# Performance work log

Hardware: AMD Instinct MI355X
Metric: run time of the kernel (lower is better)

## Reference

```python
import jax, jax.numpy as jnp
import numpy as np

NUM_SAMPLES = 4096
TAU = 0.07
EPS = 1e-20


def setup_inputs() -> dict:
    key = jax.random.key(0)
    flows = jax.random.normal(key, (32, 2, 512, 512), dtype=jnp.float32)
    return {"flows": flows}


def reference(flows):
    # flows: [b, 2, h, w]
    b, _, h, w = flows.shape
    hw = h * w
    # sampling weights: L2 norm over the 2 flow components, scaled by 1/tau
    dist = jnp.sqrt(jnp.sum(flows * flows, axis=1)) / TAU  # [b, h, w]
    dist = dist.reshape(b, hw)  # [b, h*w]
    # torch.multinomial(dist, k) without replacement == Gumbel-top-k on log-weights
    logits = jnp.log(dist + EPS)
    g = jax.random.gumbel(jax.random.key(42), (b, hw), dtype=flows.dtype)
    _, indices = jax.lax.top_k(logits + g, NUM_SAMPLES)  # [b, num_samples] int32
    # scatter-based mask (equivalent to one_hot(indices).max(dim=1), without the
    # huge [b, num_samples, h*w] intermediate)
    batch_idx = jnp.arange(b)[:, None]  # [b, 1]
    flat_masks = jnp.zeros((b, hw), dtype=flows.dtype).at[batch_idx, indices].set(1.0)
    masks = flat_masks.reshape(b, 1, h, w)  # [b, 1, h, w]
    sparse_output = masks * flows  # [b, 2, h, w]
    sparse_output = jnp.concatenate([sparse_output, masks], axis=1)  # [b, 3, h, w]
    return sparse_output, indices, masks
```

## Files before the change

kernel.cpp:

```cpp
#include <hip/hip_runtime.h>
#include <stdint.h>

#define HW 262144
#define NB 32
#define TOPK 4096
#define NTOTAL (NB * HW)
#define GBLK 4096
#define CBLK 32768

#define OUT_BYTES 134742016ull

#define OFF_WIN 33554432
#define OFF_HA  35651584
#define OFF_HB  37748736
#define OFF_STA 39845888
#define OFF_STT 39846144
#define OFF_FLG 39846272
#define OFF_CNT 39846400

__device__ __forceinline__ uint32_t rotl32(uint32_t x, int d) {
  return (x << d) | (x >> (32 - d));
}

__device__ __forceinline__ void threefry2x32_k42(uint32_t x0, uint32_t x1,
                                                 uint32_t& o0, uint32_t& o1) {
  const uint32_t ks0 = 0u;
  const uint32_t ks1 = 42u;
  const uint32_t ks2 = 0x1BD11BDAu ^ 0u ^ 42u;
  x0 += ks0;
  x1 += ks1;
#define TF_ROUND(r) { x0 += x1; x1 = rotl32(x1, (r)); x1 ^= x0; }
  TF_ROUND(13) TF_ROUND(15) TF_ROUND(26) TF_ROUND(6)
  x0 += ks1; x1 += ks2 + 1u;
  TF_ROUND(17) TF_ROUND(29) TF_ROUND(16) TF_ROUND(24)
  x0 += ks2; x1 += ks0 + 2u;
  TF_ROUND(13) TF_ROUND(15) TF_ROUND(26) TF_ROUND(6)
  x0 += ks0; x1 += ks1 + 3u;
  TF_ROUND(17) TF_ROUND(29) TF_ROUND(16) TF_ROUND(24)
  x0 += ks1; x1 += ks2 + 4u;
  TF_ROUND(13) TF_ROUND(15) TF_ROUND(26) TF_ROUND(6)
  x0 += ks2; x1 += ks0 + 5u;
#undef TF_ROUND
  o0 = x0;
  o1 = x1;
}

__device__ __forceinline__ float eigen_plogf(float xin) {
#pragma clang fp contract(off)
  uint32_t ux = __float_as_uint(xin);
  int e_int = (int)(ux >> 23) - 126;
  float x = __uint_as_float((ux & 0x007fffffu) | 0x3f000000u);
  float e = (float)e_int;
  const float SQRTHF = 0.707106781186547524f;
  bool m = (x < SQRTHF);
  float tmp = m ? x : 0.0f;
  x = x - 1.0f;
  e = e - (m ? 1.0f : 0.0f);
  x = x + tmp;
  float x2 = x * x;
  float x3 = x2 * x;
  float y  = fmaf(7.0376836292e-2f,  x, -1.1514610310e-1f);
  float y1 = fmaf(-1.2420140846e-1f, x,  1.4249322787e-1f);
  float y2 = fmaf(2.0000714765e-1f,  x, -2.4999993993e-1f);
  y  = fmaf(y,  x,  1.1676998740e-1f);
  y1 = fmaf(y1, x, -1.6668057665e-1f);
  y2 = fmaf(y2, x,  3.3333331174e-1f);
  y  = fmaf(y,  x3, y1);
  y  = fmaf(y,  x3, y2);
  y  = y * x3;
  float ey1 = e * -2.12194440e-4f;
  float t2  = x2 * 0.5f;
  y = y + ey1;
  x = x - t2;
  float ey2 = e * 0.693359375f;
  x = x + y;
  x = x + ey2;
  return x;
}

__device__ __forceinline__ float np_logf(float xin) {
#pragma clang fp contract(off)
  uint32_t ux = __float_as_uint(xin);
  int e2 = (int)(ux >> 23) - 127;
  float mant = __uint_as_float((ux & 0x007fffffu) | 0x3f800000u);
  if (mant >= 1.5f) { mant = mant * 0.5f; e2 += 1; }
  float e = (float)e2;
  float t = mant - 1.0f;
  float num = fmaf(2.589979117907922693523e-02f, t, 3.808837741388407920751e-01f);
  num = fmaf(num, t, 1.480000633400055983228e+00f);
  num = fmaf(num, t, 2.112677543073053063722e+00f);
  num = fmaf(num, t, 9.999999999999998702752e-01f);
  num = num * t;
  float den = fmaf(5.875095403124574342950e-03f, t, 1.546476374983906719538e-01f);
  den = fmaf(den, t, 9.864942958519418960339e-01f);
  den = fmaf(den, t, 2.453006071784736363091e+00f);
  den = fmaf(den, t, 2.612677543073109236779e+00f);
  den = fmaf(den, t, 1.0f);
  float r = num / den;
  return fmaf(e, 0.693147182464599609375f, r);
}

__device__ __forceinline__ uint32_t order_key(const float* __restrict__ flows,
                                              int p, uint32_t bits) {
#pragma clang fp contract(off)
  int b = p >> 18;
  int j = p & (HW - 1);
  const float* fb = flows + ((size_t)b << 19);
  float x = fb[j];
  float y = fb[j + HW];
  float xx = x * x;
  float yy = y * y;
  float ss = xx + yy;
  float sq = (float)sqrt((double)ss);
  float dist = (float)((double)sq / (double)0.07f);
  float logits = np_logf(dist + 1e-20f);
  float f = __uint_as_float((bits >> 9) | 0x3f800000u) - 1.0f;
  float u = fmaxf(f, 1.17549435e-38f);
  float g = -eigen_plogf(-eigen_plogf(u));
  float s = logits + g;
  uint32_t mm = __float_as_uint(s);
  mm = (mm & 0x80000000u) ? ~mm : (mm | 0x80000000u);
  return ~mm;
}

__global__ __launch_bounds__(1024) void k_compute(const float* __restrict__ flows,
                                                  uint32_t* __restrict__ d,
                                                  uint32_t* __restrict__ histA) {
  __shared__ uint32_t lh[16384];
  for (int i = threadIdx.x; i < 16384; i += 1024) lh[i] = 0u;
  __syncthreads();
  int base = blockIdx.x * CBLK;
  int b = base >> 18;
  for (int it = 0; it < CBLK / 1024; ++it) {
    int p = base + it * 1024 + threadIdx.x;
    uint32_t o0, o1;
    threefry2x32_k42(0u, (uint32_t)p, o0, o1);
    uint32_t dv = order_key(flows, p, o0 ^ o1);
    d[p] = dv;
    atomicAdd(&lh[dv >> 18], 1u);
  }
  __syncthreads();
  uint32_t* hb = histA + ((uint32_t)b << 14);
  for (int i = threadIdx.x; i < 16384; i += 1024) {
    uint32_t c = lh[i];
    if (c) atomicAdd(&hb[i], c);
  }
}

__global__ __launch_bounds__(1024) void k_scanA(const uint32_t* __restrict__ histA,
                                                uint32_t* __restrict__ stateA,
                                                uint32_t* __restrict__ stateT,
                                                uint32_t* __restrict__ flag) {
  int b = blockIdx.x;
  const uint32_t* h = histA + ((uint32_t)b << 14);
  int base = threadIdx.x * 16;
  uint32_t s = 0;
  for (int i = 0; i < 16; ++i) s += h[base + i];
  __shared__ uint32_t ls[1024];
  ls[threadIdx.x] = s;
  __syncthreads();
  for (int off = 1; off < 1024; off <<= 1) {
    uint32_t v = (threadIdx.x >= off) ? ls[threadIdx.x - off] : 0u;
    __syncthreads();
    ls[threadIdx.x] += v;
    __syncthreads();
  }
  uint32_t incl = ls[threadIdx.x];
  uint32_t excl = incl - s;
  if (excl < TOPK && TOPK <= incl) {
    uint32_t cum = excl;
    for (int i = 0; i < 16; ++i) {
      uint32_t c = h[base + i];
      if (cum + c >= TOPK) {
        uint32_t B = (uint32_t)(base + i);
        stateA[2 * b] = B;
        stateA[2 * b + 1] = TOPK - cum;
        stateT[b] = (B << 18) | 0x3FFFFu;
        flag[b] = (cum + c > 8192u) ? 1u : 0u;
        break;
      }
      cum += c;
    }
  }
}

__global__ __launch_bounds__(256) void k_histB(const uint32_t* __restrict__ d,
                                               const uint32_t* __restrict__ stateA,
                                               const uint32_t* __restrict__ flag,
                                               uint32_t* __restrict__ histB) {
  int base = blockIdx.x * GBLK;
  int b = base >> 18;
  if (flag[b] == 0u) return;
  uint32_t B = stateA[2 * b];
  for (int it = 0; it < GBLK / 256; ++it) {
    int p = base + it * 256 + threadIdx.x;
    uint32_t dv = d[p];
    if ((dv >> 18) == B)
      atomicAdd(&histB[((uint32_t)b << 14) + ((dv >> 4) & 0x3FFFu)], 1u);
  }
}

__global__ __launch_bounds__(1024) void k_scanB(const uint32_t* __restrict__ histB,
                                                const uint32_t* __restrict__ stateA,
                                                const uint32_t* __restrict__ flag,
                                                uint32_t* __restrict__ stateT) {
  int b = blockIdx.x;
  if (flag[b] == 0u) return;
  const uint32_t* h = histB + ((uint32_t)b << 14);
  uint32_t target = stateA[2 * b + 1];
  uint32_t B = stateA[2 * b];
  int base = threadIdx.x * 16;
  uint32_t s = 0;
  for (int i = 0; i < 16; ++i) s += h[base + i];
  __shared__ uint32_t ls[1024];
  ls[threadIdx.x] = s;
  __syncthreads();
  for (int off = 1; off < 1024; off <<= 1) {
    uint32_t v = (threadIdx.x >= off) ? ls[threadIdx.x - off] : 0u;
    __syncthreads();
    ls[threadIdx.x] += v;
    __syncthreads();
  }
  uint32_t incl = ls[threadIdx.x];
  uint32_t excl = incl - s;
  if (excl < target && target <= incl) {
    uint32_t cum = excl;
    for (int i = 0; i < 16; ++i) {
      uint32_t c = h[base + i];
      if (cum + c >= target) {
        stateT[b] = (B << 18) | ((uint32_t)(base + i) << 4) | 0xFu;
        break;
      }
      cum += c;
    }
  }
}

__global__ __launch_bounds__(256) void k_gather(const uint32_t* __restrict__ d,
                                                const uint32_t* __restrict__ stateT,
                                                uint32_t* __restrict__ cnt,
                                                unsigned long long* __restrict__ winners) {
  __shared__ unsigned long long buf[GBLK];
  __shared__ uint32_t lcnt;
  __shared__ uint32_t gbase;
  int base = blockIdx.x * GBLK;
  int b = base >> 18;
  uint32_t T = stateT[b];
  if (threadIdx.x == 0) lcnt = 0u;
  __syncthreads();
  for (int it = 0; it < GBLK / 256; ++it) {
    int p = base + it * 256 + threadIdx.x;
    uint32_t dv = d[p];
    if (dv <= T) {
      uint32_t pos = atomicAdd(&lcnt, 1u);
      buf[pos] = ((unsigned long long)dv << 32) |
                 (unsigned long long)(p & (HW - 1));
    }
  }
  __syncthreads();
  uint32_t n = lcnt;
  if (threadIdx.x == 0 && n) gbase = atomicAdd(&cnt[b], n);
  __syncthreads();
  for (uint32_t i = threadIdx.x; i < n; i += 256) {
    uint32_t pos = gbase + i;
    if (pos < 8192u) winners[(size_t)b * 8192 + pos] = buf[i];
  }
}

__global__ __launch_bounds__(256) void k_sort1(const uint32_t* __restrict__ cnt,
                                               unsigned long long* __restrict__ winners) {
  __shared__ unsigned long long s[1024];
  int blk = blockIdx.x;
  int b = blk >> 3;
  int c = blk & 7;
  uint32_t n = cnt[b];
  if (n > 8192u) n = 8192u;
  int goff = b * 8192 + c * 1024;
  for (int l = threadIdx.x; l < 1024; l += 256)
    s[l] = ((uint32_t)(c * 1024 + l) < n) ? winners[goff + l]
                                          : 0xFFFFFFFFFFFFFFFFull;
  __syncthreads();
  for (int k = 2; k <= 1024; k <<= 1) {
    for (int j = k >> 1; j > 0; j >>= 1) {
      for (int i = threadIdx.x; i < 1024; i += 256) {
        int ixj = i ^ j;
        if (ixj > i) {
          bool up = ((i & k) == 0);
          unsigned long long a = s[i];
          unsigned long long cc = s[ixj];
          if ((a > cc) == up) { s[i] = cc; s[ixj] = a; }
        }
      }
      __syncthreads();
    }
  }
  for (int l = threadIdx.x; l < 1024; l += 256) winners[goff + l] = s[l];
}

__global__ __launch_bounds__(1024) void k_rank(const unsigned long long* __restrict__ winners,
                                               const float* __restrict__ flows,
                                               float* __restrict__ out0,
                                               float* __restrict__ out_idx,
                                               float* __restrict__ out_masks) {
  __shared__ unsigned long long s[8192];
  int b = blockIdx.x;
  for (int i = threadIdx.x; i < 8192; i += 1024)
    s[i] = winners[(size_t)b * 8192 + i];
  __syncthreads();
  const float* fb = flows + ((size_t)b << 19);
  for (int i = threadIdx.x; i < 8192; i += 1024) {
    unsigned long long w = s[i];
    if (w == 0xFFFFFFFFFFFFFFFFull) continue;
    int rank = i & 1023;
    int myc = i >> 10;
    for (int c = 0; c < 8; ++c) {
      if (c == myc) continue;
      int lo = 0, hi = 1024;
      while (lo < hi) {
        int mid = (lo + hi) >> 1;
        if (s[(c << 10) + mid] < w) lo = mid + 1; else hi = mid;
      }
      rank += lo;
    }
    if (rank < TOPK) {
      uint32_t idx = (uint32_t)(w & 0xFFFFFFFFull);
      out_idx[(size_t)b * TOPK + rank] = (float)idx;
      float x = fb[idx];
      float y = fb[idx + HW];
      size_t o = ((size_t)b * 3) * HW + idx;
      out0[o] = x;
      out0[o + HW] = y;
      out0[o + 2 * HW] = 1.0f;
      out_masks[(size_t)b * HW + idx] = 1.0f;
    }
  }
}

extern "C" void kernel_launch(void* const* d_in, const int* in_sizes, int n_in,
                              void* d_out, int out_size, void* d_ws, size_t ws_size,
                              hipStream_t stream) {
  const float* flows = (const float*)d_in[0];
  float* out = (float*)d_out;
  char* ws = (char*)d_ws;

  uint32_t* d = (uint32_t*)ws;
  unsigned long long* winners = (unsigned long long*)(ws + OFF_WIN);
  uint32_t* histA = (uint32_t*)(ws + OFF_HA);
  uint32_t* histB = (uint32_t*)(ws + OFF_HB);
  uint32_t* stateA = (uint32_t*)(ws + OFF_STA);
  uint32_t* stateT = (uint32_t*)(ws + OFF_STT);
  uint32_t* flag = (uint32_t*)(ws + OFF_FLG);
  uint32_t* cnt = (uint32_t*)(ws + OFF_CNT);

  float* out_idx = out + (size_t)NB * 3 * HW;
  float* out_masks = out_idx + (size_t)NB * TOPK;

  (void)hipMemsetAsync(d_out, 0, OUT_BYTES, stream);
  (void)hipMemsetAsync(ws + OFF_HA, 0, 4194304 + 1024, stream);

  k_compute<<<NTOTAL / CBLK, 1024, 0, stream>>>(flows, d, histA);
  k_scanA<<<NB, 1024, 0, stream>>>(histA, stateA, stateT, flag);
  k_histB<<<NTOTAL / GBLK, 256, 0, stream>>>(d, stateA, flag, histB);
  k_scanB<<<NB, 1024, 0, stream>>>(histB, stateA, flag, stateT);
  k_gather<<<NTOTAL / GBLK, 256, 0, stream>>>(d, stateT, cnt, winners);
  k_sort1<<<NB * 8, 256, 0, stream>>>(cnt, winners);
  k_rank<<<NB, 1024, 0, stream>>>(winners, flows, out, out_idx, out_masks);
}
```

Baseline: 342.3 us.

## Fuse radix scan/histB/scanB kernels and fold output zeroing into gather

```diff
diff --git a/kernel.cpp b/kernel.cpp
--- a/kernel.cpp
+++ b/kernel.cpp
@@ -8,7 +8,10 @@
 #define GBLK 4096
 #define CBLK 32768
 
-#define OUT_BYTES 134742016ull
+#define OUT_F4 8421376u
+#define GTHREADS 524288u
+
+typedef float f32x4 __attribute__((ext_vector_type(4)));
 
 #define OFF_WIN 33554432
 #define OFF_HA  35651584
@@ -147,91 +150,85 @@
   }
 }
 
-__global__ __launch_bounds__(1024) void k_scanA(const uint32_t* __restrict__ histA,
-                                                uint32_t* __restrict__ stateA,
-                                                uint32_t* __restrict__ stateT,
-                                                uint32_t* __restrict__ flag) {
+__global__ __launch_bounds__(1024) void k_scanAB(const uint32_t* __restrict__ histA,
+                                                 const uint32_t* __restrict__ d,
+                                                 uint32_t* __restrict__ histB,
+                                                 uint32_t* __restrict__ stateA,
+                                                 uint32_t* __restrict__ stateT,
+                                                 uint32_t* __restrict__ flag) {
+  __shared__ uint32_t ls[1024];
+  __shared__ uint32_t bc[3];
   int b = blockIdx.x;
-  const uint32_t* h = histA + ((uint32_t)b << 14);
-  int base = threadIdx.x * 16;
-  uint32_t s = 0;
-  for (int i = 0; i < 16; ++i) s += h[base + i];
-  __shared__ uint32_t ls[1024];
-  ls[threadIdx.x] = s;
-  __syncthreads();
-  for (int off = 1; off < 1024; off <<= 1) {
-    uint32_t v = (threadIdx.x >= off) ? ls[threadIdx.x - off] : 0u;
+  {
+    const uint32_t* h = histA + ((uint32_t)b << 14);
+    int base = threadIdx.x * 16;
+    uint32_t s = 0;
+    for (int i = 0; i < 16; ++i) s += h[base + i];
+    ls[threadIdx.x] = s;
     __syncthreads();
-    ls[threadIdx.x] += v;
+    for (int off = 1; off < 1024; off <<= 1) {
+      uint32_t v = (threadIdx.x >= off) ? ls[threadIdx.x - off] : 0u;
+      __syncthreads();
+      ls[threadIdx.x] += v;
+      __syncthreads();
+    }
+    uint32_t incl = ls[threadIdx.x];
+    uint32_t excl = incl - s;
+    if (excl < TOPK && TOPK <= incl) {
+      uint32_t cum = excl;
+      for (int i = 0; i < 16; ++i) {
+        uint32_t c = h[base + i];
+        if (cum + c >= TOPK) {
+          uint32_t B = (uint32_t)(base + i);
+          stateA[2 * b] = B;
+          stateA[2 * b + 1] = TOPK - cum;
+          stateT[b] = (B << 18) | 0x3FFFFu;
+          uint32_t ov = (cum + c > 8192u) ? 1u : 0u;
+          flag[b] = ov;
+          bc[0] = B; bc[1] = TOPK - cum; bc[2] = ov;
+          break;
+        }
+        cum += c;
+      }
+    }
+  }
+  __syncthreads();
+  if (bc[2] == 0u) return;
+  uint32_t B = bc[0];
+  uint32_t target = bc[1];
+  uint32_t* h2 = histB + ((uint32_t)b << 14);
+  const uint32_t* db = d + ((size_t)b << 18);
+  for (int it = 0; it < HW / 1024; ++it) {
+    uint32_t dv = db[it * 1024 + threadIdx.x];
+    if ((dv >> 18) == B)
+      atomicAdd(&h2[(dv >> 4) & 0x3FFFu], 1u);
+  }
+  __threadfence();
+  __syncthreads();
+  {
+    int base = threadIdx.x * 16;
+    uint32_t s = 0;
+    for (int i = 0; i < 16; ++i) s += h2[base + i];
+    ls[threadIdx.x] = s;
     __syncthreads();
-  }
-  uint32_t incl = ls[threadIdx.x];
-  uint32_t excl = incl - s;
-  if (excl < TOPK && TOPK <= incl) {
-    uint32_t cum = excl;
-    for (int i = 0; i < 16; ++i) {
-      uint32_t c = h[base + i];
-      if (cum + c >= TOPK) {
-        uint32_t B = (uint32_t)(base + i);
-        stateA[2 * b] = B;
-        stateA[2 * b + 1] = TOPK - cum;
-        stateT[b] = (B << 18) | 0x3FFFFu;
-        flag[b] = (cum + c > 8192u) ? 1u : 0u;
-        break;
+    for (int off = 1; off < 1024; off <<= 1) {
+      uint32_t v = (threadIdx.x >= off) ? ls[threadIdx.x - off] : 0u;
+      __syncthreads();
+      ls[threadIdx.x] += v;
+      __syncthreads();
+    }
+    uint32_t incl = ls[threadIdx.x];
+    uint32_t excl = incl - s;
+    if (excl < target && target <= incl) {
+      uint32_t cum = excl;
+      for (int i = 0; i < 16; ++i) {
+        uint32_t c = h2[base + i];
+        if (cum + c >= target) {
+          stateT[b] = (B << 18) | ((uint32_t)(base + i) << 4) | 0xFu;
+          break;
+        }
+        cum += c;
       }
-      cum += c;
-    }
-  }
-}
-
-__global__ __launch_bounds__(256) void k_histB(const uint32_t* __restrict__ d,
-                                               const uint32_t* __restrict__ stateA,
-                                               const uint32_t* __restrict__ flag,
-                                               uint32_t* __restrict__ histB) {
-  int base = blockIdx.x * GBLK;
-  int b = base >> 18;
-  if (flag[b] == 0u) return;
-  uint32_t B = stateA[2 * b];
-  for (int it = 0; it < GBLK / 256; ++it) {
-    int p = base + it * 256 + threadIdx.x;
-    uint32_t dv = d[p];
-    if ((dv >> 18) == B)
-      atomicAdd(&histB[((uint32_t)b << 14) + ((dv >> 4) & 0x3FFFu)], 1u);
-  }
-}
-
-__global__ __launch_bounds__(1024) void k_scanB(const uint32_t* __restrict__ histB,
-                                                const uint32_t* __restrict__ stateA,
-                                                const uint32_t* __restrict__ flag,
-                                                uint32_t* __restrict__ stateT) {
-  int b = blockIdx.x;
-  if (flag[b] == 0u) return;
-  const uint32_t* h = histB + ((uint32_t)b << 14);
-  uint32_t target = stateA[2 * b + 1];
-  uint32_t B = stateA[2 * b];
-  int base = threadIdx.x * 16;
-  uint32_t s = 0;
-  for (int i = 0; i < 16; ++i) s += h[base + i];
-  __shared__ uint32_t ls[1024];
-  ls[threadIdx.x] = s;
-  __syncthreads();
-  for (int off = 1; off < 1024; off <<= 1) {
-    uint32_t v = (threadIdx.x >= off) ? ls[threadIdx.x - off] : 0u;
-    __syncthreads();
-    ls[threadIdx.x] += v;
-    __syncthreads();
-  }
-  uint32_t incl = ls[threadIdx.x];
-  uint32_t excl = incl - s;
-  if (excl < target && target <= incl) {
-    uint32_t cum = excl;
-    for (int i = 0; i < 16; ++i) {
-      uint32_t c = h[base + i];
-      if (cum + c >= target) {
-        stateT[b] = (B << 18) | ((uint32_t)(base + i) << 4) | 0xFu;
-        break;
-      }
-      cum += c;
     }
   }
 }
@@ -239,24 +236,30 @@
 __global__ __launch_bounds__(256) void k_gather(const uint32_t* __restrict__ d,
                                                 const uint32_t* __restrict__ stateT,
                                                 uint32_t* __restrict__ cnt,
-                                                unsigned long long* __restrict__ winners) {
+                                                unsigned long long* __restrict__ winners,
+                                                f32x4* __restrict__ outz) {
   __shared__ unsigned long long buf[GBLK];
   __shared__ uint32_t lcnt;
   __shared__ uint32_t gbase;
   int base = blockIdx.x * GBLK;
   int b = base >> 18;
   uint32_t T = stateT[b];
+  uint32_t gt = (uint32_t)blockIdx.x * 256u + threadIdx.x;
+  const f32x4 z4 = {0.f, 0.f, 0.f, 0.f};
   if (threadIdx.x == 0) lcnt = 0u;
   __syncthreads();
   for (int it = 0; it < GBLK / 256; ++it) {
     int p = base + it * 256 + threadIdx.x;
     uint32_t dv = d[p];
+    outz[(uint32_t)it * GTHREADS + gt] = z4;
     if (dv <= T) {
       uint32_t pos = atomicAdd(&lcnt, 1u);
       buf[pos] = ((unsigned long long)dv << 32) |
                  (unsigned long long)(p & (HW - 1));
     }
   }
+  { uint32_t z = 16u * GTHREADS + gt;
+    if (z < OUT_F4) outz[z] = z4; }
   __syncthreads();
   uint32_t n = lcnt;
   if (threadIdx.x == 0 && n) gbase = atomicAdd(&cnt[b], n);
@@ -355,14 +358,12 @@
   float* out_idx = out + (size_t)NB * 3 * HW;
   float* out_masks = out_idx + (size_t)NB * TOPK;
 
-  (void)hipMemsetAsync(d_out, 0, OUT_BYTES, stream);
   (void)hipMemsetAsync(ws + OFF_HA, 0, 4194304 + 1024, stream);
 
   k_compute<<<NTOTAL / CBLK, 1024, 0, stream>>>(flows, d, histA);
-  k_scanA<<<NB, 1024, 0, stream>>>(histA, stateA, stateT, flag);
-  k_histB<<<NTOTAL / GBLK, 256, 0, stream>>>(d, stateA, flag, histB);
-  k_scanB<<<NB, 1024, 0, stream>>>(histB, stateA, flag, stateT);
-  k_gather<<<NTOTAL / GBLK, 256, 0, stream>>>(d, stateT, cnt, winners);
+  k_scanAB<<<NB, 1024, 0, stream>>>(histA, d, histB, stateA, stateT, flag);
+  k_gather<<<NTOTAL / GBLK, 256, 0, stream>>>(d, stateT, cnt, winners,
+                                              (f32x4*)out);
   k_sort1<<<NB * 8, 256, 0, stream>>>(cnt, winners);
   k_rank<<<NB, 1024, 0, stream>>>(winners, flows, out, out_idx, out_masks);
 }
```

After: 327.0 us. -4.5%, faster.
